# Kernel optimization log

Measured on AMD Instinct MI355X. Metric: run time of the kernel, lower is better.

## Reference

```python
import jax, jax.numpy as jnp
import numpy as np

B, D_IN, HID, DIM, M = 4096, 128, 200, 256, 32
SIGMA, OMEGA = 1.0, 1.7
LB, UB = 0.0, 1.0


def setup_inputs() -> dict:
    key = jax.random.key(0)
    ks = jax.random.split(key, 9)
    s = lambda d: 1.0 / jnp.sqrt(jnp.float32(d))
    return {
        "x": jax.random.normal(ks[0], (B, D_IN), jnp.float32),
        "b": jax.random.uniform(ks[1], (B, M), jnp.float32),
        "W1": jax.random.normal(ks[2], (D_IN, HID), jnp.float32) * s(D_IN),
        "b1": jnp.zeros((HID,), jnp.float32),
        "W2": jax.random.normal(ks[3], (HID, HID), jnp.float32) * s(HID),
        "b2": jnp.zeros((HID,), jnp.float32),
        "W3": jax.random.normal(ks[4], (HID, DIM), jnp.float32) * s(HID),
        "b3": jnp.zeros((DIM,), jnp.float32),
        "A": jax.random.normal(ks[5], (M, DIM), jnp.float32) * s(DIM),
        "step": 1000,
        "n_iter": 100,
    }


def reference(x, b, W1, b1, W2, b2, W3, b3, A, step, n_iter):
    # --- MLP: Dense(200) -> relu -> Dense(200) -> relu -> Dense(dim) ---
    h = jax.nn.relu(x @ W1 + b1)
    h = jax.nn.relu(h @ W2 + b2)
    y = h @ W3 + b3  # [B, DIM]

    # schedule = linear_schedule(0.0, 0.0, ...) -> alpha == 0.0 always
    alpha = jnp.float32(0.0)

    # --- projection onto {z : A z = b, LB <= z <= UB} via relaxed
    # Douglas-Rachford / SOR fixed-point iteration (sigma/omega) ---
    AAt_inv = jnp.linalg.inv(A @ A.T + 1e-6 * jnp.eye(M, dtype=A.dtype))

    def p_aff(z):  # affine equality projection, z: [B, DIM]
        r = z @ A.T - b            # [B, M] residual
        return z - (r @ AAt_inv) @ A

    def p_box(z):
        return jnp.clip(z, LB, UB)

    def body(z, _):
        u = p_aff(z)
        v = p_box(2.0 * u - z)     # reflection then box projection
        z = z + SIGMA * OMEGA * (v - u)
        return z, None

    z0 = y  # project.get_init(x): initialize fixed point at MLP output
    z_final, _ = jax.lax.scan(body, z0, None, length=n_iter)
    proj = p_aff(z_final)

    # interpolation between raw MLP output and projection (alpha == 0)
    out = alpha * y + (1.0 - alpha) * proj
    return out
```

## Files before the change

### kernel.cpp

```cpp
#include <hip/hip_runtime.h>
#include <hip/hip_bf16.h>

typedef float    f4v    __attribute__((ext_vector_type(4)));
typedef short    short8 __attribute__((ext_vector_type(8)));
typedef unsigned u2v    __attribute__((ext_vector_type(2)));

constexpr int Bn = 4096, TR = 16;

__device__ inline unsigned cvt2(float x, float y) {
  union { __hip_bfloat162 h; unsigned u; } c;
  c.h = __float22bfloat162_rn(float2{x, y});
  return c.u;
}
__device__ inline void split_pair(float x, float y, unsigned& hp, unsigned& lp) {
  hp = cvt2(x, y);
  float hx = __uint_as_float(hp << 16);
  float hy = __uint_as_float(hp & 0xffff0000u);
  lp = cvt2(x - hx, y - hy);
}
union S8U { unsigned u[4]; short8 s; };
__device__ inline void split8(const float v[8], short8& hi, short8& lo) {
  S8U h, l;
  #pragma unroll
  for (int d = 0; d < 4; ++d) split_pair(v[2 * d], v[2 * d + 1], h.u[d], l.u[d]);
  hi = h.s; lo = l.s;
}
__device__ inline void split8p(const float* p, short8& hi, short8& lo) {
  f4v a = *(const f4v*)p, b = *(const f4v*)(p + 4);
  float v[8] = {a[0], a[1], a[2], a[3], b[0], b[1], b[2], b[3]};
  split8(v, hi, lo);
}
__device__ inline f4v mfma16(short8 a, short8 b, f4v c) {
  return __builtin_amdgcn_mfma_f32_16x16x32_bf16(a, b, c, 0, 0, 0);
}
__device__ __attribute__((always_inline)) inline f4v gdot8(
    const short8 (&ah)[8], const short8 (&al)[8],
    const short8 (&bh)[8], const short8 (&bl)[8]) {
  f4v c = {0.f, 0.f, 0.f, 0.f};
  #pragma unroll
  for (int s = 0; s < 8; ++s) {
    c = mfma16(ah[s], bh[s], c);
    c = mfma16(al[s], bh[s], c);
    c = mfma16(ah[s], bl[s], c);
  }
  return c;
}

__global__ __launch_bounds__(256) void k_prep(const float* __restrict__ A,
                                              float* __restrict__ KAT) {
  __shared__ __align__(16) float As[32 * 256];
  __shared__ float Gm[32 * 68];
  __shared__ float GinvL[32 * 32];

  const int t = threadIdx.x;
  const int lane = t & 63, wv = t >> 6, quad = lane >> 4, l15 = lane & 15;
  const int T = wv & 1, kh = wv >> 1;

  for (int i = t; i < 2048; i += 256)
    ((f4v*)As)[i] = ((const f4v*)A)[i];
  __syncthreads();

  {
    short8 afh[2][8], afl[2][8];
    #pragma unroll
    for (int tt = 0; tt < 2; ++tt)
      #pragma unroll
      for (int s = 0; s < 8; ++s)
        split8p(As + (l15 + 16 * tt) * 256 + 32 * s + 8 * quad,
                afh[tt][s], afl[tt][s]);
    f4v cg;
    if      (wv == 0) cg = gdot8(afh[0], afl[0], afh[0], afl[0]);
    else if (wv == 1) cg = gdot8(afh[1], afl[1], afh[0], afl[0]);
    else if (wv == 2) cg = gdot8(afh[0], afl[0], afh[1], afl[1]);
    else              cg = gdot8(afh[1], afl[1], afh[1], afl[1]);
    #pragma unroll
    for (int r = 0; r < 4; ++r) {
      int gi = 16 * T + 4 * quad + r, gj = 16 * kh + l15;
      Gm[gi * 68 + gj]      = cg[r] + (gi == gj ? 1e-6f : 0.f);
      Gm[gi * 68 + 32 + gj] = (gi == gj) ? 1.f : 0.f;
    }
  }
  __syncthreads();

  if (wv == 0) {
    float gcol[32];
    #pragma unroll
    for (int i = 0; i < 32; ++i) gcol[i] = Gm[i * 68 + lane];
    #pragma unroll
    for (int k = 0; k < 32; ++k) {
      float ckk  = __shfl(gcol[k], k);
      float ipiv = 1.f / ckk;
      float pivj = gcol[k] * ipiv;
      gcol[k] = pivj;
      #pragma unroll
      for (int i = 0; i < 32; ++i) {
        if (i == k) continue;
        float cki = __shfl(gcol[i], k);
        gcol[i] = fmaf(-cki, pivj, gcol[i]);
      }
    }
    if (lane >= 32) {
      #pragma unroll
      for (int i = 0; i < 32; ++i) GinvL[i * 32 + (lane - 32)] = gcol[i];
    }
  }
  __syncthreads();

  {
    float res[32];
    #pragma unroll
    for (int m = 0; m < 32; ++m) res[m] = 0.f;
    for (int p = 0; p < 32; ++p) {
      float av = As[p * 256 + t];
      #pragma unroll
      for (int m4 = 0; m4 < 8; ++m4) {
        f4v g = *(const f4v*)&GinvL[p * 32 + 4 * m4];
        res[4 * m4 + 0] = fmaf(av, g[0], res[4 * m4 + 0]);
        res[4 * m4 + 1] = fmaf(av, g[1], res[4 * m4 + 1]);
        res[4 * m4 + 2] = fmaf(av, g[2], res[4 * m4 + 2]);
        res[4 * m4 + 3] = fmaf(av, g[3], res[4 * m4 + 3]);
      }
    }
    #pragma unroll
    for (int m4 = 0; m4 < 8; ++m4) {
      f4v v = {res[4 * m4], res[4 * m4 + 1], res[4 * m4 + 2], res[4 * m4 + 3]};
      *(f4v*)&KAT[t * 32 + 4 * m4] = v;
    }
  }
}

__global__ __launch_bounds__(512, 1) void k_main(
    const float* __restrict__ x,  const float* __restrict__ bmat,
    const float* __restrict__ W1, const float* __restrict__ b1,
    const float* __restrict__ W2, const float* __restrict__ b2,
    const float* __restrict__ W3, const float* __restrict__ b3,
    const float* __restrict__ A,  const float* __restrict__ KAT,
    const int* __restrict__ n_iter_p, float* __restrict__ out) {

  __shared__ __align__(16) float    ubuf[8768];
  __shared__ __align__(16) unsigned zfrag[4096];
  __shared__ __align__(16) unsigned rfrag[512];

  const int t = threadIdx.x;
  const int lane = t & 63, wv = t >> 6, quad = lane >> 4, l15 = lane & 15;
  const int row0 = blockIdx.x * TR;

  float* xs = ubuf;
  float* h1 = ubuf + 2112;
  float* h2 = ubuf + 5440;
  float* ys = ubuf;

  if (t < 512) {
    int r = t >> 5, c4 = t & 31;
    *(f4v*)&xs[r * 132 + 4 * c4] = *(const f4v*)&x[(size_t)(row0 + r) * 128 + 4 * c4];
  }
  __syncthreads();

  {
    const int rg = wv, oc = lane;
    const bool g3 = (oc < 8);
    float acc[4][2];

    #pragma unroll
    for (int oi = 0; oi < 4; ++oi) { acc[oi][0] = 0.f; acc[oi][1] = 0.f; }
    for (int k4 = 0; k4 < 32; ++k4) {
      f4v xv0 = *(const f4v*)&xs[(2 * rg + 0) * 132 + 4 * k4];
      f4v xv1 = *(const f4v*)&xs[(2 * rg + 1) * 132 + 4 * k4];
      #pragma unroll
      for (int kk = 0; kk < 4; ++kk) {
        const float* wr = W1 + (4 * k4 + kk) * 200 + oc;
        float w0 = wr[0], w1c = wr[64], w2c = wr[128];
        float w3c = g3 ? wr[192] : 0.f;
        acc[0][0] = fmaf(xv0[kk], w0, acc[0][0]);  acc[0][1] = fmaf(xv1[kk], w0, acc[0][1]);
        acc[1][0] = fmaf(xv0[kk], w1c, acc[1][0]); acc[1][1] = fmaf(xv1[kk], w1c, acc[1][1]);
        acc[2][0] = fmaf(xv0[kk], w2c, acc[2][0]); acc[2][1] = fmaf(xv1[kk], w2c, acc[2][1]);
        acc[3][0] = fmaf(xv0[kk], w3c, acc[3][0]); acc[3][1] = fmaf(xv1[kk], w3c, acc[3][1]);
      }
    }
    #pragma unroll
    for (int oi = 0; oi < 4; ++oi) {
      if (oi == 3 && !g3) continue;
      float bb = b1[oc + 64 * oi];
      h1[(2 * rg + 0) * 208 + oc + 64 * oi] = fmaxf(acc[oi][0] + bb, 0.f);
      h1[(2 * rg + 1) * 208 + oc + 64 * oi] = fmaxf(acc[oi][1] + bb, 0.f);
    }
    __syncthreads();

    #pragma unroll
    for (int oi = 0; oi < 4; ++oi) { acc[oi][0] = 0.f; acc[oi][1] = 0.f; }
    for (int k4 = 0; k4 < 50; ++k4) {
      f4v xv0 = *(const f4v*)&h1[(2 * rg + 0) * 208 + 4 * k4];
      f4v xv1 = *(const f4v*)&h1[(2 * rg + 1) * 208 + 4 * k4];
      #pragma unroll
      for (int kk = 0; kk < 4; ++kk) {
        const float* wr = W2 + (4 * k4 + kk) * 200 + oc;
        float w0 = wr[0], w1c = wr[64], w2c = wr[128];
        float w3c = g3 ? wr[192] : 0.f;
        acc[0][0] = fmaf(xv0[kk], w0, acc[0][0]);  acc[0][1] = fmaf(xv1[kk], w0, acc[0][1]);
        acc[1][0] = fmaf(xv0[kk], w1c, acc[1][0]); acc[1][1] = fmaf(xv1[kk], w1c, acc[1][1]);
        acc[2][0] = fmaf(xv0[kk], w2c, acc[2][0]); acc[2][1] = fmaf(xv1[kk], w2c, acc[2][1]);
        acc[3][0] = fmaf(xv0[kk], w3c, acc[3][0]); acc[3][1] = fmaf(xv1[kk], w3c, acc[3][1]);
      }
    }
    #pragma unroll
    for (int oi = 0; oi < 4; ++oi) {
      if (oi == 3 && !g3) continue;
      float bb = b2[oc + 64 * oi];
      h2[(2 * rg + 0) * 208 + oc + 64 * oi] = fmaxf(acc[oi][0] + bb, 0.f);
      h2[(2 * rg + 1) * 208 + oc + 64 * oi] = fmaxf(acc[oi][1] + bb, 0.f);
    }
    __syncthreads();

    #pragma unroll
    for (int oi = 0; oi < 4; ++oi) { acc[oi][0] = 0.f; acc[oi][1] = 0.f; }
    for (int k4 = 0; k4 < 50; ++k4) {
      f4v xv0 = *(const f4v*)&h2[(2 * rg + 0) * 208 + 4 * k4];
      f4v xv1 = *(const f4v*)&h2[(2 * rg + 1) * 208 + 4 * k4];
      #pragma unroll
      for (int kk = 0; kk < 4; ++kk) {
        const float* wr = W3 + (4 * k4 + kk) * 256 + oc;
        float w0 = wr[0], w1c = wr[64], w2c = wr[128], w3c = wr[192];
        acc[0][0] = fmaf(xv0[kk], w0, acc[0][0]);  acc[0][1] = fmaf(xv1[kk], w0, acc[0][1]);
        acc[1][0] = fmaf(xv0[kk], w1c, acc[1][0]); acc[1][1] = fmaf(xv1[kk], w1c, acc[1][1]);
        acc[2][0] = fmaf(xv0[kk], w2c, acc[2][0]); acc[2][1] = fmaf(xv1[kk], w2c, acc[2][1]);
        acc[3][0] = fmaf(xv0[kk], w3c, acc[3][0]); acc[3][1] = fmaf(xv1[kk], w3c, acc[3][1]);
      }
    }
    __syncthreads();
    #pragma unroll
    for (int oi = 0; oi < 4; ++oi) {
      float bb = b3[oc + 64 * oi];
      ys[(2 * rg + 0) * 260 + oc + 64 * oi] = acc[oi][0] + bb;
      ys[(2 * rg + 1) * 260 + oc + 64 * oi] = acc[oi][1] + bb;
    }
  }
  __syncthreads();

  const int T = wv;
  short8 aah[8], aal[8];
  f4v binit = {0.f, 0.f, 0.f, 0.f};
  if (wv < 2) {
    #pragma unroll
    for (int s = 0; s < 8; ++s) {
      const float* ap = A + (size_t)(l15 + 16 * T) * 256 + 32 * s + 8 * quad;
      float v[8];
      #pragma unroll
      for (int j = 0; j < 8; ++j) v[j] = ap[j];
      split8(v, aah[s], aal[s]);
    }
    f4v bv = *(const f4v*)&bmat[(size_t)(row0 + l15) * 32 + 16 * T + 4 * quad];
    binit = -bv;
  }

  short8 kanh[2], kanl[2];
  #pragma unroll
  for (int u = 0; u < 2; ++u) {
    const int U = 2 * wv + u;
    const float* kp = KAT + (size_t)(16 * U + l15) * 32 + 8 * quad;
    float v[8];
    #pragma unroll
    for (int j = 0; j < 8; ++j) v[j] = kp[j];
    split8(v, kanh[u], kanl[u]);
  }

  int zoff[2];
  #pragma unroll
  for (int u = 0; u < 2; ++u) {
    const int U = 2 * wv + u;
    const int qp = 2 * (U & 1) + (quad >> 1);
    zoff[u] = (((U >> 3) * 4 + ((U >> 1) & 3)) * 2) * 256
              + qp * 64 + l15 * 4 + 2 * (quad & 1);
  }

  float zr[2][4];
  #pragma unroll
  for (int u = 0; u < 2; ++u) {
    const int U = 2 * wv + u;
    f4v yv = *(const f4v*)&ys[l15 * 260 + 16 * U + 4 * quad];
    #pragma unroll
    for (int r = 0; r < 4; ++r) zr[u][r] = yv[r];
    unsigned h0, l0, h1_, l1_;
    split_pair(zr[u][0], zr[u][1], h0, l0);
    split_pair(zr[u][2], zr[u][3], h1_, l1_);
    u2v hv; hv[0] = h0; hv[1] = h1_;
    u2v lv; lv[0] = l0; lv[1] = l1_;
    *(u2v*)&zfrag[zoff[u]] = hv;
    *(u2v*)&zfrag[zoff[u] + 256] = lv;
  }
  __syncthreads();

  const int niter = n_iter_p[0];

  for (int it = 0; it <= niter; ++it) {
    if (wv < 2) {
      short8 zfh[8], zfl[8];
      #pragma unroll
      for (int s = 0; s < 8; ++s) {
        zfh[s] = *(const short8*)&zfrag[(s * 2 + 0) * 256 + lane * 4];
        zfl[s] = *(const short8*)&zfrag[(s * 2 + 1) * 256 + lane * 4];
      }
      f4v c0 = binit;
      f4v c1 = {0.f, 0.f, 0.f, 0.f};
      f4v c2 = {0.f, 0.f, 0.f, 0.f};
      f4v c3 = {0.f, 0.f, 0.f, 0.f};
      #pragma unroll
      for (int s4 = 0; s4 < 2; ++s4) {
        int s = 4 * s4;
        c0 = mfma16(aah[s+0], zfh[s+0], c0);
        c1 = mfma16(aah[s+1], zfh[s+1], c1);
        c2 = mfma16(aah[s+2], zfh[s+2], c2);
        c3 = mfma16(aah[s+3], zfh[s+3], c3);
        c0 = mfma16(aal[s+0], zfh[s+0], c0);
        c1 = mfma16(aal[s+1], zfh[s+1], c1);
        c2 = mfma16(aal[s+2], zfh[s+2], c2);
        c3 = mfma16(aal[s+3], zfh[s+3], c3);
        c0 = mfma16(aah[s+0], zfl[s+0], c0);
        c1 = mfma16(aah[s+1], zfl[s+1], c1);
        c2 = mfma16(aah[s+2], zfl[s+2], c2);
        c3 = mfma16(aah[s+3], zfl[s+3], c3);
      }
      f4v rA = (c0 + c1) + (c2 + c3);
      unsigned h0, l0, h1_, l1_;
      split_pair(rA[0], rA[1], h0, l0);
      split_pair(rA[2], rA[3], h1_, l1_);
      const int rb = (2 * T + (quad >> 1)) * 64 + l15 * 4 + 2 * (quad & 1);
      u2v hv; hv[0] = h0; hv[1] = h1_;
      u2v lv; lv[0] = l0; lv[1] = l1_;
      *(u2v*)&rfrag[rb] = hv;
      *(u2v*)&rfrag[rb + 256] = lv;
    }
    __syncthreads();

    const short8 rh = *(const short8*)&rfrag[0 * 256 + lane * 4];
    const short8 rl = *(const short8*)&rfrag[1 * 256 + lane * 4];
    f4v cB[2];
    #pragma unroll
    for (int u = 0; u < 2; ++u) {
      f4v cc = {0.f, 0.f, 0.f, 0.f};
      cc = mfma16(kanh[u], rh, cc);
      cc = mfma16(kanl[u], rh, cc);
      cc = mfma16(kanh[u], rl, cc);
      cB[u] = cc;
    }

    if (it < niter) {
      #pragma unroll
      for (int u = 0; u < 2; ++u) {
        #pragma unroll
        for (int r = 0; r < 4; ++r) {
          float z = zr[u][r], wvv = cB[u][r];
          float vv = fminf(fmaxf(z - 2.f * wvv, 0.f), 1.f);
          zr[u][r] = fmaf(1.7f, vv - z + wvv, z);
        }
        unsigned h0, l0, h1_, l1_;
        split_pair(zr[u][0], zr[u][1], h0, l0);
        split_pair(zr[u][2], zr[u][3], h1_, l1_);
        u2v hv; hv[0] = h0; hv[1] = h1_;
        u2v lv; lv[0] = l0; lv[1] = l1_;
        *(u2v*)&zfrag[zoff[u]] = hv;
        *(u2v*)&zfrag[zoff[u] + 256] = lv;
      }
      __syncthreads();
    } else {
      #pragma unroll
      for (int u = 0; u < 2; ++u) {
        const int U = 2 * wv + u;
        f4v ov;
        #pragma unroll
        for (int r = 0; r < 4; ++r) ov[r] = zr[u][r] - cB[u][r];
        *(f4v*)&out[(size_t)(row0 + l15) * 256 + 16 * U + 4 * quad] = ov;
      }
    }
  }
}

extern "C" void kernel_launch(void* const* d_in, const int* in_sizes, int n_in,
                              void* d_out, int out_size, void* d_ws, size_t ws_size,
                              hipStream_t stream) {
  const float* x    = (const float*)d_in[0];
  const float* bmat = (const float*)d_in[1];
  const float* W1   = (const float*)d_in[2];
  const float* b1   = (const float*)d_in[3];
  const float* W2   = (const float*)d_in[4];
  const float* b2   = (const float*)d_in[5];
  const float* W3   = (const float*)d_in[6];
  const float* b3   = (const float*)d_in[7];
  const float* A    = (const float*)d_in[8];
  const int*  n_it  = (const int*)d_in[10];
  float* KAT = (float*)d_ws;
  float* out = (float*)d_out;

  hipLaunchKernelGGL(k_prep, dim3(1), dim3(256), 0, stream, A, KAT);
  hipLaunchKernelGGL(k_main, dim3(Bn / TR), dim3(512), 0, stream,
                     x, bmat, W1, b1, W2, b2, W3, b3, A, KAT, n_it, out);
}
```

Before: 218.3 us.

## Precompute dense projector matrix to fuse affine projection into one GEMM per iteration

Adds a prep kernel that forms Q = I - KAT·A (the full 256x256 affine projector), split into bf16 hi/lo parts, plus a per-row constant K·b. The iteration then computes u = Q z + c with a single 3-pass MFMA chain, replacing the two-stage residual and back-projection with its intermediate LDS round-trip and extra barrier. It also double-buffers the z fragments to remove one sync, and halves the block to 256 threads with 4 rows per wave in the MLP. The cost is 8x more MFMA work per iteration (256x256 instead of 2x32x256) and many more registers for the Q fragments.

```diff
diff --git a/kernel.cpp b/kernel.cpp
--- a/kernel.cpp
+++ b/kernel.cpp
@@ -44,6 +44,16 @@
     c = mfma16(ah[s], bl[s], c);
   }
   return c;
+}
+
+__device__ inline void pack_write(unsigned* dst, float z0, float z1, float z2, float z3) {
+  unsigned a0, b0, a1, b1;
+  split_pair(z0, z1, a0, b0);
+  split_pair(z2, z3, a1, b1);
+  u2v hv; hv[0] = a0; hv[1] = a1;
+  u2v lv; lv[0] = b0; lv[1] = b1;
+  *(u2v*)&dst[0]   = hv;
+  *(u2v*)&dst[256] = lv;
 }
 
 __global__ __launch_bounds__(256) void k_prep(const float* __restrict__ A,
@@ -129,17 +139,48 @@
   }
 }
 
-__global__ __launch_bounds__(512, 1) void k_main(
+__global__ __launch_bounds__(256) void k_prep2(const float* __restrict__ A,
+                                               const float* __restrict__ KAT,
+                                               unsigned* __restrict__ QTH,
+                                               unsigned* __restrict__ QTL) {
+  const int t = threadIdx.x, lane = t & 63, wv = t >> 6;
+  const int n = blockIdx.x * 4 + wv;
+  const int k0 = lane * 4;
+  const float* kr = KAT + n * 32;
+  f4v p = {0.f, 0.f, 0.f, 0.f};
+  #pragma unroll
+  for (int m = 0; m < 32; ++m) {
+    float km = kr[m];
+    f4v av = *(const f4v*)&A[m * 256 + k0];
+    p[0] = fmaf(km, av[0], p[0]);
+    p[1] = fmaf(km, av[1], p[1]);
+    p[2] = fmaf(km, av[2], p[2]);
+    p[3] = fmaf(km, av[3], p[3]);
+  }
+  float q0 = ((k0 + 0) == n ? 1.f : 0.f) - p[0];
+  float q1 = ((k0 + 1) == n ? 1.f : 0.f) - p[1];
+  float q2 = ((k0 + 2) == n ? 1.f : 0.f) - p[2];
+  float q3 = ((k0 + 3) == n ? 1.f : 0.f) - p[3];
+  unsigned a0, b0, a1, b1;
+  split_pair(q0, q1, a0, b0);
+  split_pair(q2, q3, a1, b1);
+  u2v hv; hv[0] = a0; hv[1] = a1;
+  u2v lv; lv[0] = b0; lv[1] = b1;
+  *(u2v*)&QTH[n * 128 + lane * 2] = hv;
+  *(u2v*)&QTL[n * 128 + lane * 2] = lv;
+}
+
+__global__ __launch_bounds__(256, 1) void k_main(
     const float* __restrict__ x,  const float* __restrict__ bmat,
     const float* __restrict__ W1, const float* __restrict__ b1,
     const float* __restrict__ W2, const float* __restrict__ b2,
     const float* __restrict__ W3, const float* __restrict__ b3,
-    const float* __restrict__ A,  const float* __restrict__ KAT,
+    const float* __restrict__ KAT,
+    const short* __restrict__ QTHs, const short* __restrict__ QTLs,
     const int* __restrict__ n_iter_p, float* __restrict__ out) {
 
   __shared__ __align__(16) float    ubuf[8768];
-  __shared__ __align__(16) unsigned zfrag[4096];
-  __shared__ __align__(16) unsigned rfrag[512];
+  __shared__ __align__(16) unsigned zfrag[8192];
 
   const int t = threadIdx.x;
   const int lane = t & 63, wv = t >> 6, quad = lane >> 4, l15 = lane & 15;
@@ -150,224 +191,213 @@
   float* h2 = ubuf + 5440;
   float* ys = ubuf;
 
-  if (t < 512) {
-    int r = t >> 5, c4 = t & 31;
+  for (int i = t; i < 512; i += 256) {
+    int r = i >> 5, c4 = i & 31;
     *(f4v*)&xs[r * 132 + 4 * c4] = *(const f4v*)&x[(size_t)(row0 + r) * 128 + 4 * c4];
   }
   __syncthreads();
 
   {
-    const int rg = wv, oc = lane;
+    const int oc = lane;
     const bool g3 = (oc < 8);
-    float acc[4][2];
-
-    #pragma unroll
-    for (int oi = 0; oi < 4; ++oi) { acc[oi][0] = 0.f; acc[oi][1] = 0.f; }
+    const int r0 = 4 * wv;
+    float acc[4][4];
+
+    #pragma unroll
+    for (int oi = 0; oi < 4; ++oi)
+      #pragma unroll
+      for (int ri = 0; ri < 4; ++ri) acc[oi][ri] = 0.f;
     for (int k4 = 0; k4 < 32; ++k4) {
-      f4v xv0 = *(const f4v*)&xs[(2 * rg + 0) * 132 + 4 * k4];
-      f4v xv1 = *(const f4v*)&xs[(2 * rg + 1) * 132 + 4 * k4];
+      f4v xv[4];
+      #pragma unroll
+      for (int ri = 0; ri < 4; ++ri) xv[ri] = *(const f4v*)&xs[(r0 + ri) * 132 + 4 * k4];
       #pragma unroll
       for (int kk = 0; kk < 4; ++kk) {
         const float* wr = W1 + (4 * k4 + kk) * 200 + oc;
         float w0 = wr[0], w1c = wr[64], w2c = wr[128];
         float w3c = g3 ? wr[192] : 0.f;
-        acc[0][0] = fmaf(xv0[kk], w0, acc[0][0]);  acc[0][1] = fmaf(xv1[kk], w0, acc[0][1]);
-        acc[1][0] = fmaf(xv0[kk], w1c, acc[1][0]); acc[1][1] = fmaf(xv1[kk], w1c, acc[1][1]);
-        acc[2][0] = fmaf(xv0[kk], w2c, acc[2][0]); acc[2][1] = fmaf(xv1[kk], w2c, acc[2][1]);
-        acc[3][0] = fmaf(xv0[kk], w3c, acc[3][0]); acc[3][1] = fmaf(xv1[kk], w3c, acc[3][1]);
+        #pragma unroll
+        for (int ri = 0; ri < 4; ++ri) {
+          float xx = xv[ri][kk];
+          acc[0][ri] = fmaf(xx, w0, acc[0][ri]);
+          acc[1][ri] = fmaf(xx, w1c, acc[1][ri]);
+          acc[2][ri] = fmaf(xx, w2c, acc[2][ri]);
+          acc[3][ri] = fmaf(xx, w3c, acc[3][ri]);
+        }
       }
     }
     #pragma unroll
     for (int oi = 0; oi < 4; ++oi) {
       if (oi == 3 && !g3) continue;
       float bb = b1[oc + 64 * oi];
-      h1[(2 * rg + 0) * 208 + oc + 64 * oi] = fmaxf(acc[oi][0] + bb, 0.f);
-      h1[(2 * rg + 1) * 208 + oc + 64 * oi] = fmaxf(acc[oi][1] + bb, 0.f);
+      #pragma unroll
+      for (int ri = 0; ri < 4; ++ri)
+        h1[(r0 + ri) * 208 + oc + 64 * oi] = fmaxf(acc[oi][ri] + bb, 0.f);
     }
     __syncthreads();
 
     #pragma unroll
-    for (int oi = 0; oi < 4; ++oi) { acc[oi][0] = 0.f; acc[oi][1] = 0.f; }
+    for (int oi = 0; oi < 4; ++oi)
+      #pragma unroll
+      for (int ri = 0; ri < 4; ++ri) acc[oi][ri] = 0.f;
     for (int k4 = 0; k4 < 50; ++k4) {
-      f4v xv0 = *(const f4v*)&h1[(2 * rg + 0) * 208 + 4 * k4];
-      f4v xv1 = *(const f4v*)&h1[(2 * rg + 1) * 208 + 4 * k4];
+      f4v xv[4];
+      #pragma unroll
+      for (int ri = 0; ri < 4; ++ri) xv[ri] = *(const f4v*)&h1[(r0 + ri) * 208 + 4 * k4];
       #pragma unroll
       for (int kk = 0; kk < 4; ++kk) {
         const float* wr = W2 + (4 * k4 + kk) * 200 + oc;
         float w0 = wr[0], w1c = wr[64], w2c = wr[128];
         float w3c = g3 ? wr[192] : 0.f;
-        acc[0][0] = fmaf(xv0[kk], w0, acc[0][0]);  acc[0][1] = fmaf(xv1[kk], w0, acc[0][1]);
-        acc[1][0] = fmaf(xv0[kk], w1c, acc[1][0]); acc[1][1] = fmaf(xv1[kk], w1c, acc[1][1]);
-        acc[2][0] = fmaf(xv0[kk], w2c, acc[2][0]); acc[2][1] = fmaf(xv1[kk], w2c, acc[2][1]);
-        acc[3][0] = fmaf(xv0[kk], w3c, acc[3][0]); acc[3][1] = fmaf(xv1[kk], w3c, acc[3][1]);
+        #pragma unroll
+        for (int ri = 0; ri < 4; ++ri) {
+          float xx = xv[ri][kk];
+          acc[0][ri] = fmaf(xx, w0, acc[0][ri]);
+          acc[1][ri] = fmaf(xx, w1c, acc[1][ri]);
+          acc[2][ri] = fmaf(xx, w2c, acc[2][ri]);
+          acc[3][ri] = fmaf(xx, w3c, acc[3][ri]);
+        }
       }
     }
     #pragma unroll
     for (int oi = 0; oi < 4; ++oi) {
       if (oi == 3 && !g3) continue;
       float bb = b2[oc + 64 * oi];
-      h2[(2 * rg + 0) * 208 + oc + 64 * oi] = fmaxf(acc[oi][0] + bb, 0.f);
-      h2[(2 * rg + 1) * 208 + oc + 64 * oi] = fmaxf(acc[oi][1] + bb, 0.f);
+      #pragma unroll
+      for (int ri = 0; ri < 4; ++ri)
+        h2[(r0 + ri) * 208 + oc + 64 * oi] = fmaxf(acc[oi][ri] + bb, 0.f);
     }
     __syncthreads();
 
     #pragma unroll
-    for (int oi = 0; oi < 4; ++oi) { acc[oi][0] = 0.f; acc[oi][1] = 0.f; }
+    for (int oi = 0; oi < 4; ++oi)
+      #pragma unroll
+      for (int ri = 0; ri < 4; ++ri) acc[oi][ri] = 0.f;
     for (int k4 = 0; k4 < 50; ++k4) {
-      f4v xv0 = *(const f4v*)&h2[(2 * rg + 0) * 208 + 4 * k4];
-      f4v xv1 = *(const f4v*)&h2[(2 * rg + 1) * 208 + 4 * k4];
+      f4v xv[4];
+      #pragma unroll
+      for (int ri = 0; ri < 4; ++ri) xv[ri] = *(const f4v*)&h2[(r0 + ri) * 208 + 4 * k4];
       #pragma unroll
       for (int kk = 0; kk < 4; ++kk) {
         const float* wr = W3 + (4 * k4 + kk) * 256 + oc;
         float w0 = wr[0], w1c = wr[64], w2c = wr[128], w3c = wr[192];
-        acc[0][0] = fmaf(xv0[kk], w0, acc[0][0]);  acc[0][1] = fmaf(xv1[kk], w0, acc[0][1]);
-        acc[1][0] = fmaf(xv0[kk], w1c, acc[1][0]); acc[1][1] = fmaf(xv1[kk], w1c, acc[1][1]);
-        acc[2][0] = fmaf(xv0[kk], w2c, acc[2][0]); acc[2][1] = fmaf(xv1[kk], w2c, acc[2][1]);
-        acc[3][0] = fmaf(xv0[kk], w3c, acc[3][0]); acc[3][1] = fmaf(xv1[kk], w3c, acc[3][1]);
+        #pragma unroll
+        for (int ri = 0; ri < 4; ++ri) {
+          float xx = xv[ri][kk];
+          acc[0][ri] = fmaf(xx, w0, acc[0][ri]);
+          acc[1][ri] = fmaf(xx, w1c, acc[1][ri]);
+          acc[2][ri] = fmaf(xx, w2c, acc[2][ri]);
+          acc[3][ri] = fmaf(xx, w3c, acc[3][ri]);
+        }
       }
     }
     __syncthreads();
     #pragma unroll
     for (int oi = 0; oi < 4; ++oi) {
       float bb = b3[oc + 64 * oi];
-      ys[(2 * rg + 0) * 260 + oc + 64 * oi] = acc[oi][0] + bb;
-      ys[(2 * rg + 1) * 260 + oc + 64 * oi] = acc[oi][1] + bb;
-    }
-  }
-  __syncthreads();
-
-  const int T = wv;
-  short8 aah[8], aal[8];
-  f4v binit = {0.f, 0.f, 0.f, 0.f};
-  if (wv < 2) {
+      #pragma unroll
+      for (int ri = 0; ri < 4; ++ri)
+        ys[(r0 + ri) * 260 + oc + 64 * oi] = acc[oi][ri] + bb;
+    }
+  }
+  __syncthreads();
+
+  short8 qh[4][8], ql[4][8];
+  #pragma unroll
+  for (int u = 0; u < 4; ++u) {
+    const int n = 16 * (4 * wv + u) + l15;
     #pragma unroll
     for (int s = 0; s < 8; ++s) {
-      const float* ap = A + (size_t)(l15 + 16 * T) * 256 + 32 * s + 8 * quad;
-      float v[8];
-      #pragma unroll
-      for (int j = 0; j < 8; ++j) v[j] = ap[j];
-      split8(v, aah[s], aal[s]);
-    }
-    f4v bv = *(const f4v*)&bmat[(size_t)(row0 + l15) * 32 + 16 * T + 4 * quad];
-    binit = -bv;
-  }
-
-  short8 kanh[2], kanl[2];
-  #pragma unroll
-  for (int u = 0; u < 2; ++u) {
-    const int U = 2 * wv + u;
-    const float* kp = KAT + (size_t)(16 * U + l15) * 32 + 8 * quad;
-    float v[8];
-    #pragma unroll
-    for (int j = 0; j < 8; ++j) v[j] = kp[j];
-    split8(v, kanh[u], kanl[u]);
-  }
-
-  int zoff[2];
-  #pragma unroll
-  for (int u = 0; u < 2; ++u) {
-    const int U = 2 * wv + u;
+      qh[u][s] = *(const short8*)&QTHs[n * 256 + 32 * s + 8 * quad];
+      ql[u][s] = *(const short8*)&QTLs[n * 256 + 32 * s + 8 * quad];
+    }
+  }
+
+  float bv[32];
+  #pragma unroll
+  for (int m4 = 0; m4 < 8; ++m4)
+    *(f4v*)&bv[4 * m4] = *(const f4v*)&bmat[(size_t)(row0 + l15) * 32 + 4 * m4];
+  f4v crv[4];
+  #pragma unroll
+  for (int u = 0; u < 4; ++u) {
+    #pragma unroll
+    for (int r = 0; r < 4; ++r) {
+      const float* kp = KAT + (size_t)(16 * (4 * wv + u) + 4 * quad + r) * 32;
+      float s = 0.f;
+      #pragma unroll
+      for (int m4 = 0; m4 < 8; ++m4) {
+        f4v kv = *(const f4v*)&kp[4 * m4];
+        s = fmaf(bv[4 * m4 + 0], kv[0], s);
+        s = fmaf(bv[4 * m4 + 1], kv[1], s);
+        s = fmaf(bv[4 * m4 + 2], kv[2], s);
+        s = fmaf(bv[4 * m4 + 3], kv[3], s);
+      }
+      crv[u][r] = s;
+    }
+  }
+
+  int zoff[4];
+  float zr[4][4];
+  #pragma unroll
+  for (int u = 0; u < 4; ++u) {
+    const int U = 4 * wv + u;
     const int qp = 2 * (U & 1) + (quad >> 1);
-    zoff[u] = (((U >> 3) * 4 + ((U >> 1) & 3)) * 2) * 256
-              + qp * 64 + l15 * 4 + 2 * (quad & 1);
-  }
-
-  float zr[2][4];
-  #pragma unroll
-  for (int u = 0; u < 2; ++u) {
-    const int U = 2 * wv + u;
+    zoff[u] = ((U >> 1) * 2) * 256 + qp * 64 + l15 * 4 + 2 * (quad & 1);
     f4v yv = *(const f4v*)&ys[l15 * 260 + 16 * U + 4 * quad];
     #pragma unroll
     for (int r = 0; r < 4; ++r) zr[u][r] = yv[r];
-    unsigned h0, l0, h1_, l1_;
-    split_pair(zr[u][0], zr[u][1], h0, l0);
-    split_pair(zr[u][2], zr[u][3], h1_, l1_);
-    u2v hv; hv[0] = h0; hv[1] = h1_;
-    u2v lv; lv[0] = l0; lv[1] = l1_;
-    *(u2v*)&zfrag[zoff[u]] = hv;
-    *(u2v*)&zfrag[zoff[u] + 256] = lv;
+    pack_write(&zfrag[zoff[u]], zr[u][0], zr[u][1], zr[u][2], zr[u][3]);
   }
   __syncthreads();
 
   const int niter = n_iter_p[0];
+  const int zrd = lane * 4;
 
   for (int it = 0; it <= niter; ++it) {
-    if (wv < 2) {
-      short8 zfh[8], zfl[8];
-      #pragma unroll
-      for (int s = 0; s < 8; ++s) {
-        zfh[s] = *(const short8*)&zfrag[(s * 2 + 0) * 256 + lane * 4];
-        zfl[s] = *(const short8*)&zfrag[(s * 2 + 1) * 256 + lane * 4];
-      }
-      f4v c0 = binit;
-      f4v c1 = {0.f, 0.f, 0.f, 0.f};
-      f4v c2 = {0.f, 0.f, 0.f, 0.f};
-      f4v c3 = {0.f, 0.f, 0.f, 0.f};
-      #pragma unroll
-      for (int s4 = 0; s4 < 2; ++s4) {
-        int s = 4 * s4;
-        c0 = mfma16(aah[s+0], zfh[s+0], c0);
-        c1 = mfma16(aah[s+1], zfh[s+1], c1);
-        c2 = mfma16(aah[s+2], zfh[s+2], c2);
-        c3 = mfma16(aah[s+3], zfh[s+3], c3);
-        c0 = mfma16(aal[s+0], zfh[s+0], c0);
-        c1 = mfma16(aal[s+1], zfh[s+1], c1);
-        c2 = mfma16(aal[s+2], zfh[s+2], c2);
-        c3 = mfma16(aal[s+3], zfh[s+3], c3);
-        c0 = mfma16(aah[s+0], zfl[s+0], c0);
-        c1 = mfma16(aah[s+1], zfl[s+1], c1);
-        c2 = mfma16(aah[s+2], zfl[s+2], c2);
-        c3 = mfma16(aah[s+3], zfl[s+3], c3);
-      }
-      f4v rA = (c0 + c1) + (c2 + c3);
-      unsigned h0, l0, h1_, l1_;
-      split_pair(rA[0], rA[1], h0, l0);
-      split_pair(rA[2], rA[3], h1_, l1_);
-      const int rb = (2 * T + (quad >> 1)) * 64 + l15 * 4 + 2 * (quad & 1);
-      u2v hv; hv[0] = h0; hv[1] = h1_;
-      u2v lv; lv[0] = l0; lv[1] = l1_;
-      *(u2v*)&rfrag[rb] = hv;
-      *(u2v*)&rfrag[rb + 256] = lv;
-    }
-    __syncthreads();
-
-    const short8 rh = *(const short8*)&rfrag[0 * 256 + lane * 4];
-    const short8 rl = *(const short8*)&rfrag[1 * 256 + lane * 4];
-    f4v cB[2];
-    #pragma unroll
-    for (int u = 0; u < 2; ++u) {
-      f4v cc = {0.f, 0.f, 0.f, 0.f};
-      cc = mfma16(kanh[u], rh, cc);
-      cc = mfma16(kanl[u], rh, cc);
-      cc = mfma16(kanh[u], rl, cc);
-      cB[u] = cc;
+    const unsigned* zb = zfrag + ((it & 1) << 12);
+    unsigned*       zw = zfrag + (((it & 1) ^ 1) << 12);
+
+    f4v uA[4], uB[4], uC[4];
+    #pragma unroll
+    for (int u = 0; u < 4; ++u) {
+      uA[u] = crv[u];
+      uB[u] = (f4v){0.f, 0.f, 0.f, 0.f};
+      uC[u] = (f4v){0.f, 0.f, 0.f, 0.f};
+    }
+    #pragma unroll
+    for (int s = 0; s < 8; ++s) {
+      short8 zh = *(const short8*)&zb[(2 * s + 0) * 256 + zrd];
+      short8 zl = *(const short8*)&zb[(2 * s + 1) * 256 + zrd];
+      #pragma unroll
+      for (int u = 0; u < 4; ++u) uA[u] = mfma16(qh[u][s], zh, uA[u]);
+      #pragma unroll
+      for (int u = 0; u < 4; ++u) uB[u] = mfma16(ql[u][s], zh, uB[u]);
+      #pragma unroll
+      for (int u = 0; u < 4; ++u) uC[u] = mfma16(qh[u][s], zl, uC[u]);
     }
 
     if (it < niter) {
       #pragma unroll
-      for (int u = 0; u < 2; ++u) {
+      for (int u = 0; u < 4; ++u) {
+        float zn[4];
         #pragma unroll
         for (int r = 0; r < 4; ++r) {
-          float z = zr[u][r], wvv = cB[u][r];
-          float vv = fminf(fmaxf(z - 2.f * wvv, 0.f), 1.f);
-          zr[u][r] = fmaf(1.7f, vv - z + wvv, z);
+          float uv = (uA[u][r] + uB[u][r]) + uC[u][r];
+          float z  = zr[u][r];
+          float vv = fminf(fmaxf(fmaf(2.f, uv, -z), 0.f), 1.f);
+          zn[r] = fmaf(1.7f, vv - uv, z);
+          zr[u][r] = zn[r];
         }
-        unsigned h0, l0, h1_, l1_;
-        split_pair(zr[u][0], zr[u][1], h0, l0);
-        split_pair(zr[u][2], zr[u][3], h1_, l1_);
-        u2v hv; hv[0] = h0; hv[1] = h1_;
-        u2v lv; lv[0] = l0; lv[1] = l1_;
-        *(u2v*)&zfrag[zoff[u]] = hv;
-        *(u2v*)&zfrag[zoff[u] + 256] = lv;
+        pack_write(&zw[zoff[u]], zn[0], zn[1], zn[2], zn[3]);
       }
       __syncthreads();
     } else {
       #pragma unroll
-      for (int u = 0; u < 2; ++u) {
-        const int U = 2 * wv + u;
+      for (int u = 0; u < 4; ++u) {
+        const int U = 4 * wv + u;
         f4v ov;
         #pragma unroll
-        for (int r = 0; r < 4; ++r) ov[r] = zr[u][r] - cB[u][r];
+        for (int r = 0; r < 4; ++r) ov[r] = (uA[u][r] + uB[u][r]) + uC[u][r];
         *(f4v*)&out[(size_t)(row0 + l15) * 256 + 16 * U + 4 * quad] = ov;
       }
     }
@@ -387,10 +417,15 @@
   const float* b3   = (const float*)d_in[7];
   const float* A    = (const float*)d_in[8];
   const int*  n_it  = (const int*)d_in[10];
-  float* KAT = (float*)d_ws;
+
+  float*    KAT = (float*)d_ws;
+  unsigned* QTH = (unsigned*)((char*)d_ws + 32768);
+  unsigned* QTL = QTH + 256 * 128;
   float* out = (float*)d_out;
 
-  hipLaunchKernelGGL(k_prep, dim3(1), dim3(256), 0, stream, A, KAT);
-  hipLaunchKernelGGL(k_main, dim3(Bn / TR), dim3(512), 0, stream,
-                     x, bmat, W1, b1, W2, b2, W3, b3, A, KAT, n_it, out);
-}
+  hipLaunchKernelGGL(k_prep,  dim3(1),       dim3(256), 0, stream, A, KAT);
+  hipLaunchKernelGGL(k_prep2, dim3(64),      dim3(256), 0, stream, A, KAT, QTH, QTL);
+  hipLaunchKernelGGL(k_main,  dim3(Bn / TR), dim3(256), 0, stream,
+                     x, bmat, W1, b1, W2, b2, W3, b3, KAT,
+                     (const short*)QTH, (const short*)QTL, n_it, out);
+}
```

Result: slower. 294.5 us (+34.9%).

## Split residual GEMM across all eight waves with double-buffered z fragments

Applied to the files above, without the earlier changes.

The A·z residual product used to run on only 2 of 8 waves. It is now split over the K dimension across all 8 waves, and partial sums go through shared memory where every wave reduces them. The z fragment buffer is double-buffered, which removes one barrier per iteration. The 1-block-per-CU launch bound hint is dropped. The change adds an fp32 partial-sum round trip through LDS and a larger LDS footprint, which may limit occupancy.

```diff
diff --git a/kernel.cpp b/kernel.cpp
--- a/kernel.cpp
+++ b/kernel.cpp
@@ -44,6 +44,16 @@
     c = mfma16(ah[s], bl[s], c);
   }
   return c;
+}
+
+__device__ inline void pack_write(unsigned* dst, float z0, float z1, float z2, float z3) {
+  unsigned a0, b0, a1, b1;
+  split_pair(z0, z1, a0, b0);
+  split_pair(z2, z3, a1, b1);
+  u2v hv; hv[0] = a0; hv[1] = a1;
+  u2v lv; lv[0] = b0; lv[1] = b1;
+  *(u2v*)&dst[0]   = hv;
+  *(u2v*)&dst[256] = lv;
 }
 
 __global__ __launch_bounds__(256) void k_prep(const float* __restrict__ A,
@@ -129,7 +139,8 @@
   }
 }
 
-__global__ __launch_bounds__(512, 1) void k_main(
+__global__ __launch_bounds__(512)
+void k_main(
     const float* __restrict__ x,  const float* __restrict__ bmat,
     const float* __restrict__ W1, const float* __restrict__ b1,
     const float* __restrict__ W2, const float* __restrict__ b2,
@@ -138,8 +149,7 @@
     const int* __restrict__ n_iter_p, float* __restrict__ out) {
 
   __shared__ __align__(16) float    ubuf[8768];
-  __shared__ __align__(16) unsigned zfrag[4096];
-  __shared__ __align__(16) unsigned rfrag[512];
+  __shared__ __align__(16) unsigned zfrag[12288];
 
   const int t = threadIdx.x;
   const int lane = t & 63, wv = t >> 6, quad = lane >> 4, l15 = lane & 15;
@@ -150,7 +160,7 @@
   float* h2 = ubuf + 5440;
   float* ys = ubuf;
 
-  if (t < 512) {
+  {
     int r = t >> 5, c4 = t & 31;
     *(f4v*)&xs[r * 132 + 4 * c4] = *(const f4v*)&x[(size_t)(row0 + r) * 128 + 4 * c4];
   }
@@ -236,18 +246,19 @@
   }
   __syncthreads();
 
-  const int T = wv;
-  short8 aah[8], aal[8];
+  const int T = wv & 1, kq = wv >> 1;
+  short8 aah[2], aal[2];
+  #pragma unroll
+  for (int ss = 0; ss < 2; ++ss) {
+    const int s = 2 * kq + ss;
+    const float* ap = A + (size_t)(l15 + 16 * T) * 256 + 32 * s + 8 * quad;
+    float v[8];
+    #pragma unroll
+    for (int j = 0; j < 8; ++j) v[j] = ap[j];
+    split8(v, aah[ss], aal[ss]);
+  }
   f4v binit = {0.f, 0.f, 0.f, 0.f};
-  if (wv < 2) {
-    #pragma unroll
-    for (int s = 0; s < 8; ++s) {
-      const float* ap = A + (size_t)(l15 + 16 * T) * 256 + 32 * s + 8 * quad;
-      float v[8];
-      #pragma unroll
-      for (int j = 0; j < 8; ++j) v[j] = ap[j];
-      split8(v, aah[s], aal[s]);
-    }
+  if (kq == 0) {
     f4v bv = *(const f4v*)&bmat[(size_t)(row0 + l15) * 32 + 16 * T + 4 * quad];
     binit = -bv;
   }
@@ -262,77 +273,61 @@
     for (int j = 0; j < 8; ++j) v[j] = kp[j];
     split8(v, kanh[u], kanl[u]);
   }
+  #pragma unroll
+  for (int ss = 0; ss < 2; ++ss)
+    asm volatile("" : "+v"(aah[ss]), "+v"(aal[ss]), "+v"(kanh[ss]), "+v"(kanl[ss]));
 
   int zoff[2];
+  float zr[2][4];
   #pragma unroll
   for (int u = 0; u < 2; ++u) {
     const int U = 2 * wv + u;
     const int qp = 2 * (U & 1) + (quad >> 1);
-    zoff[u] = (((U >> 3) * 4 + ((U >> 1) & 3)) * 2) * 256
-              + qp * 64 + l15 * 4 + 2 * (quad & 1);
-  }
-
-  float zr[2][4];
-  #pragma unroll
-  for (int u = 0; u < 2; ++u) {
-    const int U = 2 * wv + u;
+    zoff[u] = ((U >> 1) * 2) * 256 + qp * 64 + l15 * 4 + 2 * (quad & 1);
     f4v yv = *(const f4v*)&ys[l15 * 260 + 16 * U + 4 * quad];
     #pragma unroll
     for (int r = 0; r < 4; ++r) zr[u][r] = yv[r];
-    unsigned h0, l0, h1_, l1_;
-    split_pair(zr[u][0], zr[u][1], h0, l0);
-    split_pair(zr[u][2], zr[u][3], h1_, l1_);
-    u2v hv; hv[0] = h0; hv[1] = h1_;
-    u2v lv; lv[0] = l0; lv[1] = l1_;
-    *(u2v*)&zfrag[zoff[u]] = hv;
-    *(u2v*)&zfrag[zoff[u] + 256] = lv;
+    pack_write(&zfrag[zoff[u]], zr[u][0], zr[u][1], zr[u][2], zr[u][3]);
   }
   __syncthreads();
 
   const int niter = n_iter_p[0];
+  const int zrd = lane * 4;
+  float* pbuf = ubuf;
+  const int pwr = ((T * 4 + kq) * 64 + lane) * 4;
+  const int Tq = quad >> 1, qs = quad & 1;
+  const int prdA = (Tq * 4 * 64 + l15 + 32 * qs) * 4;
 
   for (int it = 0; it <= niter; ++it) {
-    if (wv < 2) {
-      short8 zfh[8], zfl[8];
-      #pragma unroll
-      for (int s = 0; s < 8; ++s) {
-        zfh[s] = *(const short8*)&zfrag[(s * 2 + 0) * 256 + lane * 4];
-        zfl[s] = *(const short8*)&zfrag[(s * 2 + 1) * 256 + lane * 4];
-      }
+    const unsigned* zb = zfrag + ((it & 1) << 12);
+    unsigned*       zw = zfrag + (((it & 1) ^ 1) << 12);
+
+    {
+      const int s0 = 2 * kq;
+      short8 zh0 = *(const short8*)&zb[(2 * s0 + 0) * 256 + zrd];
+      short8 zl0 = *(const short8*)&zb[(2 * s0 + 1) * 256 + zrd];
+      short8 zh1 = *(const short8*)&zb[(2 * s0 + 2) * 256 + zrd];
+      short8 zl1 = *(const short8*)&zb[(2 * s0 + 3) * 256 + zrd];
       f4v c0 = binit;
       f4v c1 = {0.f, 0.f, 0.f, 0.f};
-      f4v c2 = {0.f, 0.f, 0.f, 0.f};
-      f4v c3 = {0.f, 0.f, 0.f, 0.f};
-      #pragma unroll
-      for (int s4 = 0; s4 < 2; ++s4) {
-        int s = 4 * s4;
-        c0 = mfma16(aah[s+0], zfh[s+0], c0);
-        c1 = mfma16(aah[s+1], zfh[s+1], c1);
-        c2 = mfma16(aah[s+2], zfh[s+2], c2);
-        c3 = mfma16(aah[s+3], zfh[s+3], c3);
-        c0 = mfma16(aal[s+0], zfh[s+0], c0);
-        c1 = mfma16(aal[s+1], zfh[s+1], c1);
-        c2 = mfma16(aal[s+2], zfh[s+2], c2);
-        c3 = mfma16(aal[s+3], zfh[s+3], c3);
-        c0 = mfma16(aah[s+0], zfl[s+0], c0);
-        c1 = mfma16(aah[s+1], zfl[s+1], c1);
-        c2 = mfma16(aah[s+2], zfl[s+2], c2);
-        c3 = mfma16(aah[s+3], zfl[s+3], c3);
-      }
-      f4v rA = (c0 + c1) + (c2 + c3);
-      unsigned h0, l0, h1_, l1_;
-      split_pair(rA[0], rA[1], h0, l0);
-      split_pair(rA[2], rA[3], h1_, l1_);
-      const int rb = (2 * T + (quad >> 1)) * 64 + l15 * 4 + 2 * (quad & 1);
-      u2v hv; hv[0] = h0; hv[1] = h1_;
-      u2v lv; lv[0] = l0; lv[1] = l1_;
-      *(u2v*)&rfrag[rb] = hv;
-      *(u2v*)&rfrag[rb + 256] = lv;
+      c0 = mfma16(aah[0], zh0, c0);  c1 = mfma16(aah[1], zh1, c1);
+      c0 = mfma16(aal[0], zh0, c0);  c1 = mfma16(aal[1], zh1, c1);
+      c0 = mfma16(aah[0], zl0, c0);  c1 = mfma16(aah[1], zl1, c1);
+      *(f4v*)&pbuf[pwr] = c0 + c1;
     }
     __syncthreads();
 
-    const short8 rh = *(const short8*)&rfrag[0 * 256 + lane * 4];
-    const short8 rl = *(const short8*)&rfrag[1 * 256 + lane * 4];
+    f4v va = {0.f, 0.f, 0.f, 0.f}, vb = {0.f, 0.f, 0.f, 0.f};
+    #pragma unroll
+    for (int k = 0; k < 4; ++k) {
+      const int base = prdA + k * 256;
+      va += *(const f4v*)&pbuf[base];
+      vb += *(const f4v*)&pbuf[base + 64];
+    }
+    float rv[8] = {va[0], va[1], va[2], va[3], vb[0], vb[1], vb[2], vb[3]};
+    short8 rh, rl;
+    split8(rv, rh, rl);
+
     f4v cB[2];
     #pragma unroll
     for (int u = 0; u < 2; ++u) {
@@ -346,19 +341,15 @@
     if (it < niter) {
       #pragma unroll
       for (int u = 0; u < 2; ++u) {
+        float zn[4];
         #pragma unroll
         for (int r = 0; r < 4; ++r) {
           float z = zr[u][r], wvv = cB[u][r];
           float vv = fminf(fmaxf(z - 2.f * wvv, 0.f), 1.f);
-          zr[u][r] = fmaf(1.7f, vv - z + wvv, z);
+          zn[r] = fmaf(1.7f, vv - z + wvv, z);
+          zr[u][r] = zn[r];
         }
-        unsigned h0, l0, h1_, l1_;
-        split_pair(zr[u][0], zr[u][1], h0, l0);
-        split_pair(zr[u][2], zr[u][3], h1_, l1_);
-        u2v hv; hv[0] = h0; hv[1] = h1_;
-        u2v lv; lv[0] = l0; lv[1] = l1_;
-        *(u2v*)&zfrag[zoff[u]] = hv;
-        *(u2v*)&zfrag[zoff[u] + 256] = lv;
+        pack_write(&zw[zoff[u]], zn[0], zn[1], zn[2], zn[3]);
       }
       __syncthreads();
     } else {
@@ -387,6 +378,7 @@
   const float* b3   = (const float*)d_in[7];
   const float* A    = (const float*)d_in[8];
   const int*  n_it  = (const int*)d_in[10];
+
   float* KAT = (float*)d_ws;
   float* out = (float*)d_out;
 
```

Result: slower. 227.1 us (+4.0%).
